# Kernel optimization log

Hardware: AMD Instinct MI355X
Metric: run time of the kernel (lower is better)

The kernel has to match this reference:

```python
import jax, jax.numpy as jnp
import numpy as np
import math

B, H, W = 32, 512, 512
BS = 8
QUALITY = 50.0  # __scale_quality(75) = 200 - 2*75


def _make_dctmtx(bs=BS):
    m = np.empty((bs, bs), dtype=np.float32)
    for j in range(bs):
        for i in range(bs):
            if i == 0:
                m[i, j] = 1.0 / math.sqrt(bs)
            else:
                m[i, j] = math.sqrt(2.0 / bs) * math.cos(math.pi * (2 * j + 1) * i / (2 * bs))
    return jnp.asarray(m)


def _make_quantize():
    qY = np.array([[16,11,10,16,24,40,51,61],[12,12,14,19,26,58,60,55],
                   [14,13,16,24,40,57,69,56],[14,17,22,29,51,87,80,62],
                   [18,22,37,56,68,109,103,77],[24,35,55,64,81,104,113,92],
                   [49,64,78,87,103,121,120,101],[72,92,95,98,112,100,103,99]], dtype=np.float32) / 255.0
    qC = np.array([[17,18,24,47,99,99,99,99],[18,21,26,66,99,99,99,99],
                   [24,26,56,99,99,99,99,99],[47,66,99,99,99,99,99,99],
                   [99,99,99,99,99,99,99,99],[99,99,99,99,99,99,99,99],
                   [99,99,99,99,99,99,99,99],[99,99,99,99,99,99,99,99]], dtype=np.float32) / 255.0
    return jnp.asarray(np.stack([qY, qC, qC], axis=0))


def setup_inputs() -> dict:
    key = jax.random.key(0)
    x = jax.random.uniform(key, (B, 3, H, W), dtype=jnp.float32)
    return {"input": x, "quantize": _make_quantize(), "dctmtx": _make_dctmtx()}


def reference(input, quantize, dctmtx):
    bs = BS
    b, c, h, w = input.shape
    dt = input.dtype
    rgb = 255.0 * input
    # rgb -> ycbcr (3x3 color transform, offset cb/cr by 128, clamp)
    xf = jnp.array([[0.299, 0.587, 0.114],
                    [-0.168735892, -0.331264108, 0.5],
                    [0.5, -0.418687589, -0.081312411]], dtype=dt)
    off = jnp.array([0.0, 128.0, 128.0], dtype=dt)[None, :, None, None]
    ycbcr = jnp.clip(jnp.einsum('bchw,kc->bkhw', rgb, xf) + off, 0.0, 255.0)
    # 2x2 chroma subsample: replace Cb/Cr by 2x2 block means (Y untouched)
    yc = ycbcr[:, :1]
    cc = ycbcr[:, 1:].reshape(b, 2, h // 2, 2, w // 2, 2)
    cm = jnp.mean(cc, axis=(3, 5), keepdims=True)
    cc = jnp.broadcast_to(cm, cc.shape).reshape(b, 2, h, w)
    sample = jnp.concatenate([yc, cc], axis=1) - 128.0
    # extract 8x8 blocks -> [b, h/bs, w/bs, 3, bs, bs]
    blocks = sample.reshape(b, 3, h // bs, bs, w // bs, bs).transpose(0, 2, 4, 1, 3, 5)
    # 2D DCT: D @ X @ D^T
    dcts = jnp.einsum('ij,bhwcjk,lk->bhwcil', dctmtx, blocks, dctmtx)
    # quality-scaled quant table (broadcasts [3,8,8] over blocks)
    q = jnp.round(jnp.clip(jnp.round((jnp.round(quantize * 255.0) * QUALITY + 50.0) / 100.0), 1.0, 255.0))
    comp = jnp.round(dcts / q)
    decomp = jnp.round(comp * jax.lax.stop_gradient(q))
    # IDCT: D^T @ X @ D
    idcts = jnp.einsum('ji,bhwcjk,kl->bhwcil', dctmtx, decomp, dctmtx)
    # merge blocks back -> [b,3,h,w]
    ycbcr2 = idcts.transpose(0, 3, 1, 4, 2, 5).reshape(b, 3, h, w) + 128.0
    # ycbcr -> rgb
    xf2 = jnp.array([[1.0, 0.0, 1.402],
                     [1.0, -0.344136286, -0.714136286],
                     [1.0, 1.772, 0.0]], dtype=dt)
    im = ycbcr2 - off
    rgb2 = jnp.clip(jnp.einsum('bchw,kc->bkhw', im, xf2), 0.0, 255.0)
    return jnp.round(rgb2) / 255.0
```

## Files before the change

kernel.cpp:

```cpp
#include <hip/hip_runtime.h>

#define IN_H 512
#define IN_W 512


__global__ __launch_bounds__(256, 2) void jpeg_kernel(
    const float* __restrict__ in, const float* __restrict__ qz,
    const float* __restrict__ dmtx, float* __restrict__ out)
{
    __shared__ __align__(16) unsigned char smem[39168];
    double*  Ys  = (double*) (smem);
    double*  CbS = (double*) (smem + 17408);
    double*  CrS = (double*) (smem + 22016);
    float*   Vt  = (float*)  (smem + 26624);
    double2* qt  = (double2*)(smem + 35328);
    double*  Dd  = (double*) (smem + 38784);
    float*   Dh  = (float*)  (smem + 39040);

    const int t   = threadIdx.x;
    const int blk = blockIdx.x;
    const int b   = blk >> 7;
    const int rr  = blk & 127;
    const int row0 = (rr >> 1) << 3;
    const int col0 = (rr & 1) << 8;
    const int chs = IN_H * IN_W;

    if (t < 192) {
        const int c = t >> 6, i = (t >> 3) & 7, l = t & 7;
        double v  = (double)qz[t];
        double t1 = rint((rint(v * 255.0) * 50.0 + 50.0) / 100.0);
        double q  = fmin(fmax(t1, 1.0), 255.0);
        qt[(c * 8 + l) * 9 + i] = make_double2(1.0 / q, q);
    }
    if (t < 32) {
        float dv = dmtx[(t >> 2) * 8 + (t & 3)];
        Dd[t] = (double)dv;
        Dh[t] = dv;
    }

    const int s  = t >> 6;
    const int c4 = t & 63;
    {
        const int base = ((b * 3) * IN_H + row0 + 2 * s) * IN_W + col0 + 4 * c4;
        float4 ra = *(const float4*)(in + base);
        float4 rb = *(const float4*)(in + base + IN_W);
        float4 ga = *(const float4*)(in + base + chs);
        float4 gb = *(const float4*)(in + base + chs + IN_W);
        float4 ba = *(const float4*)(in + base + 2 * chs);
        float4 bb = *(const float4*)(in + base + 2 * chs + IN_W);

        float rA[2][4] = {{ra.x,ra.y,ra.z,ra.w},{rb.x,rb.y,rb.z,rb.w}};
        float gA[2][4] = {{ga.x,ga.y,ga.z,ga.w},{gb.x,gb.y,gb.z,gb.w}};
        float bA[2][4] = {{ba.x,ba.y,ba.z,ba.w},{bb.x,bb.y,bb.z,bb.w}};

        double yv[2][4], cbv[2][4], crv[2][4];
        #pragma unroll
        for (int p = 0; p < 2; ++p) {
            #pragma unroll
            for (int k = 0; k < 4; ++k) {
                double R = 255.0 * (double)rA[p][k];
                double G = 255.0 * (double)gA[p][k];
                double B = 255.0 * (double)bA[p][k];
                double y  =  0.299*R + 0.587*G + 0.114*B;
                double cb = -0.168735892*R - 0.331264108*G + 0.5*B + 128.0;
                double cr =  0.5*R - 0.418687589*G - 0.081312411*B + 128.0;
                yv[p][k]  = fmin(fmax(y , 0.0), 255.0) - 128.0;
                cbv[p][k] = fmin(fmax(cb, 0.0), 255.0);
                crv[p][k] = fmin(fmax(cr, 0.0), 255.0);
            }
        }
        const int tile = c4 >> 1, half = c4 & 1;
        #pragma unroll
        for (int p = 0; p < 2; ++p) {
            double* yp = &Ys[tile * 68 + (2*s + p) * 8 + 4 * half];
            *(double2*)(yp)     = make_double2(yv[p][0], yv[p][1]);
            *(double2*)(yp + 2) = make_double2(yv[p][2], yv[p][3]);
        }
        double m0 = (cbv[0][0]+cbv[0][1]+cbv[1][0]+cbv[1][1])*0.25 - 128.0;
        double m1 = (cbv[0][2]+cbv[0][3]+cbv[1][2]+cbv[1][3])*0.25 - 128.0;
        *(double2*)&CbS[tile * 18 + s * 4 + 2 * half] = make_double2(m0, m1);
        double n0 = (crv[0][0]+crv[0][1]+crv[1][0]+crv[1][1])*0.25 - 128.0;
        double n1 = (crv[0][2]+crv[0][3]+crv[1][2]+crv[1][3])*0.25 - 128.0;
        *(double2*)&CrS[tile * 18 + s * 4 + 2 * half] = make_double2(n0, n1);
    }
    __syncthreads();

    const int q8 = t >> 3;
    const int l  = t & 7;
    double dl0, dl1, dl2, dl3;
    {
        double2 dA = *(const double2*)&Dd[l * 4];
        double2 dB = *(const double2*)&Dd[l * 4 + 2];
        dl0 = dA.x; dl1 = dA.y; dl2 = dB.x; dl3 = dB.y;
    }
    const double sgn  = (l & 1) ? -1.0 : 1.0;
    const double dl01 = dl0 + dl1, dl23 = dl2 + dl3;
    const float4* dh4p = (const float4*)Dh;
    float4 d0 = dh4p[0], d1 = dh4p[1], d2 = dh4p[2], d3 = dh4p[3];
    float4 d4 = dh4p[4], d5 = dh4p[5], d6 = dh4p[6], d7 = dh4p[7];

    float acc[3][8];
    float* vtw = &Vt[q8 * 68];

    #pragma unroll
    for (int c = 0; c < 3; ++c) {
        double e2[4], o2[4];
        if (c == 0) {
            const double* base = &Ys[q8 * 68];
            #pragma unroll
            for (int m = 0; m < 4; ++m) {
                double tp[2];
                #pragma unroll
                for (int h = 0; h < 2; ++h) {
                    const double* p = base + (h ? (7 - m) : m) * 8;
                    double2 a0 = *(const double2*)(p);
                    double2 a1 = *(const double2*)(p + 2);
                    double2 a2 = *(const double2*)(p + 4);
                    double2 a3 = *(const double2*)(p + 6);
                    double v0 = fma(sgn, a3.y, a0.x);
                    double v1 = fma(sgn, a3.x, a0.y);
                    double v2 = fma(sgn, a2.y, a1.x);
                    double v3 = fma(sgn, a2.x, a1.y);
                    tp[h] = dl0*v0 + dl1*v1 + dl2*v2 + dl3*v3;
                }
                e2[m] = tp[0] + tp[1];
                o2[m] = tp[0] - tp[1];
            }
        } else {
            const double* base = ((c == 1) ? CbS : CrS) + q8 * 18;
            double u4[4];
            #pragma unroll
            for (int j2 = 0; j2 < 4; ++j2) {
                double2 a0 = *(const double2*)(base + j2 * 4);
                double2 a1 = *(const double2*)(base + j2 * 4 + 2);
                u4[j2] = dl01 * fma(sgn, a1.y, a0.x) + dl23 * fma(sgn, a1.x, a0.y);
            }
            e2[0] = e2[1] = u4[0] + u4[3];  o2[0] = o2[1] = u4[0] - u4[3];
            e2[2] = e2[3] = u4[1] + u4[2];  o2[2] = o2[3] = u4[1] - u4[2];
        }

        float zo[8];
        {
            const double2* dd2  = (const double2*)Dd;
            const double2* qrow = &qt[(c * 8 + l) * 9];
            #pragma unroll
            for (int i = 0; i < 8; ++i) {
                double2 dA = dd2[i * 2], dB = dd2[i * 2 + 1];
                double a64 = (i & 1)
                    ? dA.x*o2[0] + dA.y*o2[1] + dB.x*o2[2] + dB.y*o2[3]
                    : dA.x*e2[0] + dA.y*e2[1] + dB.x*e2[2] + dB.y*e2[3];
                double2 qe = qrow[i];
                zo[i] = (float)(rint(a64 * qe.x) * qe.y);
            }
        }

        float u[8];
        {
            float se0 = zo[0]*d0.x + zo[2]*d2.x + zo[4]*d4.x + zo[6]*d6.x;
            float se1 = zo[0]*d0.y + zo[2]*d2.y + zo[4]*d4.y + zo[6]*d6.y;
            float se2 = zo[0]*d0.z + zo[2]*d2.z + zo[4]*d4.z + zo[6]*d6.z;
            float se3 = zo[0]*d0.w + zo[2]*d2.w + zo[4]*d4.w + zo[6]*d6.w;
            float so0 = zo[1]*d1.x + zo[3]*d3.x + zo[5]*d5.x + zo[7]*d7.x;
            float so1 = zo[1]*d1.y + zo[3]*d3.y + zo[5]*d5.y + zo[7]*d7.y;
            float so2 = zo[1]*d1.z + zo[3]*d3.z + zo[5]*d5.z + zo[7]*d7.z;
            float so3 = zo[1]*d1.w + zo[3]*d3.w + zo[5]*d5.w + zo[7]*d7.w;
            u[0]=se0+so0; u[7]=se0-so0;
            u[1]=se1+so1; u[6]=se1-so1;
            u[2]=se2+so2; u[5]=se2-so2;
            u[3]=se3+so3; u[4]=se3-so3;
        }

        #pragma unroll
        for (int x = 0; x < 8; ++x) vtw[x * 8 + l] = u[x];
        __builtin_amdgcn_wave_barrier();
        float w2[8];
        {
            const float* vr = vtw + l * 8;
            float4 wa = *(const float4*)(vr);
            float4 wb = *(const float4*)(vr + 4);
            w2[0]=wa.x; w2[1]=wa.y; w2[2]=wa.z; w2[3]=wa.w;
            w2[4]=wb.x; w2[5]=wb.y; w2[6]=wb.z; w2[7]=wb.w;
        }
        __builtin_amdgcn_wave_barrier();

        {
            float re0 = w2[0]*d0.x + w2[2]*d2.x + w2[4]*d4.x + w2[6]*d6.x;
            float re1 = w2[0]*d0.y + w2[2]*d2.y + w2[4]*d4.y + w2[6]*d6.y;
            float re2 = w2[0]*d0.z + w2[2]*d2.z + w2[4]*d4.z + w2[6]*d6.z;
            float re3 = w2[0]*d0.w + w2[2]*d2.w + w2[4]*d4.w + w2[6]*d6.w;
            float ro0 = w2[1]*d1.x + w2[3]*d3.x + w2[5]*d5.x + w2[7]*d7.x;
            float ro1 = w2[1]*d1.y + w2[3]*d3.y + w2[5]*d5.y + w2[7]*d7.y;
            float ro2 = w2[1]*d1.z + w2[3]*d3.z + w2[5]*d5.z + w2[7]*d7.z;
            float ro3 = w2[1]*d1.w + w2[3]*d3.w + w2[5]*d5.w + w2[7]*d7.w;
            acc[c][0]=re0+ro0; acc[c][7]=re0-ro0;
            acc[c][1]=re1+ro1; acc[c][6]=re1-ro1;
            acc[c][2]=re2+ro2; acc[c][5]=re2-ro2;
            acc[c][3]=re3+ro3; acc[c][4]=re3-ro3;
        }
    }

    {
        const int obase = ((b * 3) * IN_H + row0 + l) * IN_W + col0 + q8 * 8;
        float R4[8], G4[8], B4[8];
        #pragma unroll
        for (int y = 0; y < 8; ++y) {
            float im0 = acc[0][y] + 128.0f;
            float im1 = acc[1][y];
            float im2 = acc[2][y];
            float R  = fminf(fmaxf(im0 + 1.402f*im2, 0.0f), 255.0f);
            float G  = fminf(fmaxf(im0 - 0.344136286f*im1 - 0.714136286f*im2, 0.0f), 255.0f);
            float Bv = fminf(fmaxf(im0 + 1.772f*im1, 0.0f), 255.0f);
            R4[y] = rintf(R)  * (1.0f/255.0f);
            G4[y] = rintf(G)  * (1.0f/255.0f);
            B4[y] = rintf(Bv) * (1.0f/255.0f);
        }
        *(float4*)(out + obase)               = make_float4(R4[0],R4[1],R4[2],R4[3]);
        *(float4*)(out + obase + 4)           = make_float4(R4[4],R4[5],R4[6],R4[7]);
        *(float4*)(out + obase + chs)         = make_float4(G4[0],G4[1],G4[2],G4[3]);
        *(float4*)(out + obase + chs + 4)     = make_float4(G4[4],G4[5],G4[6],G4[7]);
        *(float4*)(out + obase + 2*chs)       = make_float4(B4[0],B4[1],B4[2],B4[3]);
        *(float4*)(out + obase + 2*chs + 4)   = make_float4(B4[4],B4[5],B4[6],B4[7]);
    }
}

extern "C" void kernel_launch(void* const* d_in, const int* in_sizes, int n_in,
                              void* d_out, int out_size, void* d_ws, size_t ws_size,
                              hipStream_t stream) {
    (void)in_sizes; (void)n_in; (void)out_size; (void)d_ws; (void)ws_size;
    const float* in  = (const float*)d_in[0];
    const float* qz  = (const float*)d_in[1];
    const float* dm  = (const float*)d_in[2];
    float* out = (float*)d_out;
    dim3 grid(4096), blk(256);
    hipLaunchKernelGGL(jpeg_kernel, grid, blk, 0, stream, in, qz, dm, out);
}
```

Baseline: 185.1 us.

## Precompute tables in a prologue kernel and load pixels per row

```diff
diff --git a/kernel.cpp b/kernel.cpp
--- a/kernel.cpp
+++ b/kernel.cpp
@@ -3,152 +3,137 @@
 #define IN_H 512
 #define IN_W 512
 
-
-__global__ __launch_bounds__(256, 2) void jpeg_kernel(
-    const float* __restrict__ in, const float* __restrict__ qz,
-    const float* __restrict__ dmtx, float* __restrict__ out)
+__global__ void jpeg_tables(const float* __restrict__ qz,
+                            const float* __restrict__ dmtx,
+                            double* __restrict__ ws)
 {
-    __shared__ __align__(16) unsigned char smem[39168];
-    double*  Ys  = (double*) (smem);
-    double*  CbS = (double*) (smem + 17408);
-    double*  CrS = (double*) (smem + 22016);
-    float*   Vt  = (float*)  (smem + 26624);
-    double2* qt  = (double2*)(smem + 35328);
-    double*  Dd  = (double*) (smem + 38784);
-    float*   Dh  = (float*)  (smem + 39040);
-
-    const int t   = threadIdx.x;
-    const int blk = blockIdx.x;
-    const int b   = blk >> 7;
-    const int rr  = blk & 127;
-    const int row0 = (rr >> 1) << 3;
-    const int col0 = (rr & 1) << 8;
-    const int chs = IN_H * IN_W;
-
+    const int t = threadIdx.x;
+    if (t < 32) ws[t] = (double)dmtx[(t >> 2) * 8 + (t & 3)];
     if (t < 192) {
         const int c = t >> 6, i = (t >> 3) & 7, l = t & 7;
         double v  = (double)qz[t];
         double t1 = rint((rint(v * 255.0) * 50.0 + 50.0) / 100.0);
         double q  = fmin(fmax(t1, 1.0), 255.0);
-        qt[(c * 8 + l) * 9 + i] = make_double2(1.0 / q, q);
-    }
-    if (t < 32) {
-        float dv = dmtx[(t >> 2) * 8 + (t & 3)];
-        Dd[t] = (double)dv;
-        Dh[t] = dv;
-    }
-
-    const int s  = t >> 6;
-    const int c4 = t & 63;
+        const int idx = (c * 8 + l) * 8 + i;
+        ws[32 + 2 * idx]     = 1.0 / q;
+        ws[32 + 2 * idx + 1] = q;
+    }
+}
+
+__global__ __launch_bounds__(256, 2) void jpeg_kernel(
+    const float* __restrict__ in, const double* __restrict__ ws,
+    float* __restrict__ out)
+{
+    __shared__ __align__(16) double Tq[32 * 68];
+    __shared__ __align__(16) float  Vt[32 * 68];
+
+    const int t    = threadIdx.x;
+    const int tile = t >> 3;
+    const int tl   = t & 7;
+    const int blk  = blockIdx.x;
+    const int b    = blk >> 7;
+    const int rr   = blk & 127;
+    const int row0 = (rr >> 1) << 3;
+    const int col0 = (rr & 1) << 8;
+    const int chs  = IN_H * IN_W;
+
+    double D[8][4];
+    #pragma unroll
+    for (int l = 0; l < 8; ++l)
+        #pragma unroll
+        for (int k = 0; k < 4; ++k) D[l][k] = ws[l * 4 + k];
+    float Dh[8][4];
+    #pragma unroll
+    for (int l = 0; l < 8; ++l)
+        #pragma unroll
+        for (int k = 0; k < 4; ++k) Dh[l][k] = (float)D[l][k];
+
+    double yv[8], hcb[4], hcr[4];
     {
-        const int base = ((b * 3) * IN_H + row0 + 2 * s) * IN_W + col0 + 4 * c4;
-        float4 ra = *(const float4*)(in + base);
-        float4 rb = *(const float4*)(in + base + IN_W);
-        float4 ga = *(const float4*)(in + base + chs);
-        float4 gb = *(const float4*)(in + base + chs + IN_W);
-        float4 ba = *(const float4*)(in + base + 2 * chs);
-        float4 bb = *(const float4*)(in + base + 2 * chs + IN_W);
-
-        float rA[2][4] = {{ra.x,ra.y,ra.z,ra.w},{rb.x,rb.y,rb.z,rb.w}};
-        float gA[2][4] = {{ga.x,ga.y,ga.z,ga.w},{gb.x,gb.y,gb.z,gb.w}};
-        float bA[2][4] = {{ba.x,ba.y,ba.z,ba.w},{bb.x,bb.y,bb.z,bb.w}};
-
-        double yv[2][4], cbv[2][4], crv[2][4];
-        #pragma unroll
-        for (int p = 0; p < 2; ++p) {
-            #pragma unroll
-            for (int k = 0; k < 4; ++k) {
-                double R = 255.0 * (double)rA[p][k];
-                double G = 255.0 * (double)gA[p][k];
-                double B = 255.0 * (double)bA[p][k];
-                double y  =  0.299*R + 0.587*G + 0.114*B;
-                double cb = -0.168735892*R - 0.331264108*G + 0.5*B + 128.0;
-                double cr =  0.5*R - 0.418687589*G - 0.081312411*B + 128.0;
-                yv[p][k]  = fmin(fmax(y , 0.0), 255.0) - 128.0;
-                cbv[p][k] = fmin(fmax(cb, 0.0), 255.0);
-                crv[p][k] = fmin(fmax(cr, 0.0), 255.0);
-            }
-        }
-        const int tile = c4 >> 1, half = c4 & 1;
-        #pragma unroll
-        for (int p = 0; p < 2; ++p) {
-            double* yp = &Ys[tile * 68 + (2*s + p) * 8 + 4 * half];
-            *(double2*)(yp)     = make_double2(yv[p][0], yv[p][1]);
-            *(double2*)(yp + 2) = make_double2(yv[p][2], yv[p][3]);
-        }
-        double m0 = (cbv[0][0]+cbv[0][1]+cbv[1][0]+cbv[1][1])*0.25 - 128.0;
-        double m1 = (cbv[0][2]+cbv[0][3]+cbv[1][2]+cbv[1][3])*0.25 - 128.0;
-        *(double2*)&CbS[tile * 18 + s * 4 + 2 * half] = make_double2(m0, m1);
-        double n0 = (crv[0][0]+crv[0][1]+crv[1][0]+crv[1][1])*0.25 - 128.0;
-        double n1 = (crv[0][2]+crv[0][3]+crv[1][2]+crv[1][3])*0.25 - 128.0;
-        *(double2*)&CrS[tile * 18 + s * 4 + 2 * half] = make_double2(n0, n1);
-    }
-    __syncthreads();
-
-    const int q8 = t >> 3;
-    const int l  = t & 7;
-    double dl0, dl1, dl2, dl3;
-    {
-        double2 dA = *(const double2*)&Dd[l * 4];
-        double2 dB = *(const double2*)&Dd[l * 4 + 2];
-        dl0 = dA.x; dl1 = dA.y; dl2 = dB.x; dl3 = dB.y;
-    }
-    const double sgn  = (l & 1) ? -1.0 : 1.0;
-    const double dl01 = dl0 + dl1, dl23 = dl2 + dl3;
-    const float4* dh4p = (const float4*)Dh;
-    float4 d0 = dh4p[0], d1 = dh4p[1], d2 = dh4p[2], d3 = dh4p[3];
-    float4 d4 = dh4p[4], d5 = dh4p[5], d6 = dh4p[6], d7 = dh4p[7];
+        const float* pin = in + ((b * 3) * IN_H + row0 + tl) * IN_W + col0 + tile * 8;
+        float4 r0 = *(const float4*)(pin);
+        float4 r1 = *(const float4*)(pin + 4);
+        float4 g0 = *(const float4*)(pin + chs);
+        float4 g1 = *(const float4*)(pin + chs + 4);
+        float4 b0 = *(const float4*)(pin + 2 * chs);
+        float4 b1 = *(const float4*)(pin + 2 * chs + 4);
+        float rf[8] = {r0.x,r0.y,r0.z,r0.w,r1.x,r1.y,r1.z,r1.w};
+        float gf[8] = {g0.x,g0.y,g0.z,g0.w,g1.x,g1.y,g1.z,g1.w};
+        float bf[8] = {b0.x,b0.y,b0.z,b0.w,b1.x,b1.y,b1.z,b1.w};
+        #pragma unroll
+        for (int k = 0; k < 8; ++k) {
+            double R = 255.0 * (double)rf[k];
+            double G = 255.0 * (double)gf[k];
+            double B = 255.0 * (double)bf[k];
+            double y  =  0.299*R + 0.587*G + 0.114*B;
+            double cb = -0.168735892*R - 0.331264108*G + 0.5*B + 128.0;
+            double cr =  0.5*R - 0.418687589*G - 0.081312411*B + 128.0;
+            yv[k] = fmin(fmax(y , 0.0), 255.0) - 128.0;
+            cb    = fmin(fmax(cb, 0.0), 255.0) - 128.0;
+            cr    = fmin(fmax(cr, 0.0), 255.0) - 128.0;
+            if ((k & 1) == 0) { hcb[k >> 1] = cb;  hcr[k >> 1] = cr; }
+            else              { hcb[k >> 1] += cb; hcr[k >> 1] += cr; }
+        }
+    }
+
+    double* tp  = &Tq[tile * 68];
+    float*  vp  = &Vt[tile * 68];
+    const double2* qtab = (const double2*)(ws + 32);
 
     float acc[3][8];
-    float* vtw = &Vt[q8 * 68];
 
     #pragma unroll
     for (int c = 0; c < 3; ++c) {
+        double e1[4], o1[4];
+        if (c == 0) {
+            #pragma unroll
+            for (int k = 0; k < 4; ++k) { e1[k] = yv[k] + yv[7-k]; o1[k] = yv[k] - yv[7-k]; }
+        } else {
+            const double* hv = (c == 1) ? hcb : hcr;
+            double A = hv[0] + hv[3], Bv = hv[1] + hv[2];
+            double C = hv[0] - hv[3], E  = hv[1] - hv[2];
+            e1[0] = A; e1[1] = A; e1[2] = Bv; e1[3] = Bv;
+            o1[0] = C; o1[1] = C; o1[2] = E;  o1[3] = E;
+        }
+        double tr[8];
+        #pragma unroll
+        for (int l = 0; l < 8; ++l) {
+            const double* s = (l & 1) ? o1 : e1;
+            tr[l] = D[l][0]*s[0] + D[l][1]*s[1] + D[l][2]*s[2] + D[l][3]*s[3];
+        }
+        #pragma unroll
+        for (int k = 0; k < 4; ++k) {
+            const int s = (2*k + 2*tl) & 7;
+            *(double2*)(tp + tl * 8 + s) = make_double2(tr[2*k], tr[2*k+1]);
+        }
+        __builtin_amdgcn_wave_barrier();
+
+        double colv[8];
+        #pragma unroll
+        for (int j = 0; j < 8; ++j) colv[j] = tp[j * 8 + ((tl + 2*j) & 7)];
+        __builtin_amdgcn_wave_barrier();
+
         double e2[4], o2[4];
         if (c == 0) {
-            const double* base = &Ys[q8 * 68];
             #pragma unroll
-            for (int m = 0; m < 4; ++m) {
-                double tp[2];
-                #pragma unroll
-                for (int h = 0; h < 2; ++h) {
-                    const double* p = base + (h ? (7 - m) : m) * 8;
-                    double2 a0 = *(const double2*)(p);
-                    double2 a1 = *(const double2*)(p + 2);
-                    double2 a2 = *(const double2*)(p + 4);
-                    double2 a3 = *(const double2*)(p + 6);
-                    double v0 = fma(sgn, a3.y, a0.x);
-                    double v1 = fma(sgn, a3.x, a0.y);
-                    double v2 = fma(sgn, a2.y, a1.x);
-                    double v3 = fma(sgn, a2.x, a1.y);
-                    tp[h] = dl0*v0 + dl1*v1 + dl2*v2 + dl3*v3;
-                }
-                e2[m] = tp[0] + tp[1];
-                o2[m] = tp[0] - tp[1];
-            }
+            for (int m = 0; m < 4; ++m) { e2[m] = colv[m] + colv[7-m]; o2[m] = colv[m] - colv[7-m]; }
         } else {
-            const double* base = ((c == 1) ? CbS : CrS) + q8 * 18;
-            double u4[4];
-            #pragma unroll
-            for (int j2 = 0; j2 < 4; ++j2) {
-                double2 a0 = *(const double2*)(base + j2 * 4);
-                double2 a1 = *(const double2*)(base + j2 * 4 + 2);
-                u4[j2] = dl01 * fma(sgn, a1.y, a0.x) + dl23 * fma(sgn, a1.x, a0.y);
-            }
-            e2[0] = e2[1] = u4[0] + u4[3];  o2[0] = o2[1] = u4[0] - u4[3];
-            e2[2] = e2[3] = u4[1] + u4[2];  o2[2] = o2[3] = u4[1] - u4[2];
+            double T0 = 0.25 * (colv[0] + colv[1]);
+            double T1 = 0.25 * (colv[2] + colv[3]);
+            double T2 = 0.25 * (colv[4] + colv[5]);
+            double T3 = 0.25 * (colv[6] + colv[7]);
+            double A = T0 + T3, Bv = T1 + T2, C = T0 - T3, E = T1 - T2;
+            e2[0] = A; e2[1] = A; e2[2] = Bv; e2[3] = Bv;
+            o2[0] = C; o2[1] = C; o2[2] = E;  o2[3] = E;
         }
 
         float zo[8];
         {
-            const double2* dd2  = (const double2*)Dd;
-            const double2* qrow = &qt[(c * 8 + l) * 9];
+            const double2* qrow = qtab + (c * 8 + tl) * 8;
             #pragma unroll
             for (int i = 0; i < 8; ++i) {
-                double2 dA = dd2[i * 2], dB = dd2[i * 2 + 1];
-                double a64 = (i & 1)
-                    ? dA.x*o2[0] + dA.y*o2[1] + dB.x*o2[2] + dB.y*o2[3]
-                    : dA.x*e2[0] + dA.y*e2[1] + dB.x*e2[2] + dB.y*e2[3];
+                const double* s = (i & 1) ? o2 : e2;
+                double a64 = D[i][0]*s[0] + D[i][1]*s[1] + D[i][2]*s[2] + D[i][3]*s[3];
                 double2 qe = qrow[i];
                 zo[i] = (float)(rint(a64 * qe.x) * qe.y);
             }
@@ -156,14 +141,14 @@
 
         float u[8];
         {
-            float se0 = zo[0]*d0.x + zo[2]*d2.x + zo[4]*d4.x + zo[6]*d6.x;
-            float se1 = zo[0]*d0.y + zo[2]*d2.y + zo[4]*d4.y + zo[6]*d6.y;
-            float se2 = zo[0]*d0.z + zo[2]*d2.z + zo[4]*d4.z + zo[6]*d6.z;
-            float se3 = zo[0]*d0.w + zo[2]*d2.w + zo[4]*d4.w + zo[6]*d6.w;
-            float so0 = zo[1]*d1.x + zo[3]*d3.x + zo[5]*d5.x + zo[7]*d7.x;
-            float so1 = zo[1]*d1.y + zo[3]*d3.y + zo[5]*d5.y + zo[7]*d7.y;
-            float so2 = zo[1]*d1.z + zo[3]*d3.z + zo[5]*d5.z + zo[7]*d7.z;
-            float so3 = zo[1]*d1.w + zo[3]*d3.w + zo[5]*d5.w + zo[7]*d7.w;
+            float se0 = zo[0]*Dh[0][0] + zo[2]*Dh[2][0] + zo[4]*Dh[4][0] + zo[6]*Dh[6][0];
+            float se1 = zo[0]*Dh[0][1] + zo[2]*Dh[2][1] + zo[4]*Dh[4][1] + zo[6]*Dh[6][1];
+            float se2 = zo[0]*Dh[0][2] + zo[2]*Dh[2][2] + zo[4]*Dh[4][2] + zo[6]*Dh[6][2];
+            float se3 = zo[0]*Dh[0][3] + zo[2]*Dh[2][3] + zo[4]*Dh[4][3] + zo[6]*Dh[6][3];
+            float so0 = zo[1]*Dh[1][0] + zo[3]*Dh[3][0] + zo[5]*Dh[5][0] + zo[7]*Dh[7][0];
+            float so1 = zo[1]*Dh[1][1] + zo[3]*Dh[3][1] + zo[5]*Dh[5][1] + zo[7]*Dh[7][1];
+            float so2 = zo[1]*Dh[1][2] + zo[3]*Dh[3][2] + zo[5]*Dh[5][2] + zo[7]*Dh[7][2];
+            float so3 = zo[1]*Dh[1][3] + zo[3]*Dh[3][3] + zo[5]*Dh[5][3] + zo[7]*Dh[7][3];
             u[0]=se0+so0; u[7]=se0-so0;
             u[1]=se1+so1; u[6]=se1-so1;
             u[2]=se2+so2; u[5]=se2-so2;
@@ -171,27 +156,26 @@
         }
 
         #pragma unroll
-        for (int x = 0; x < 8; ++x) vtw[x * 8 + l] = u[x];
+        for (int x = 0; x < 8; ++x) vp[x * 8 + tl] = u[x];
         __builtin_amdgcn_wave_barrier();
         float w2[8];
         {
-            const float* vr = vtw + l * 8;
-            float4 wa = *(const float4*)(vr);
-            float4 wb = *(const float4*)(vr + 4);
+            float4 wa = *(const float4*)(vp + tl * 8);
+            float4 wb = *(const float4*)(vp + tl * 8 + 4);
             w2[0]=wa.x; w2[1]=wa.y; w2[2]=wa.z; w2[3]=wa.w;
             w2[4]=wb.x; w2[5]=wb.y; w2[6]=wb.z; w2[7]=wb.w;
         }
         __builtin_amdgcn_wave_barrier();
 
         {
-            float re0 = w2[0]*d0.x + w2[2]*d2.x + w2[4]*d4.x + w2[6]*d6.x;
-            float re1 = w2[0]*d0.y + w2[2]*d2.y + w2[4]*d4.y + w2[6]*d6.y;
-            float re2 = w2[0]*d0.z + w2[2]*d2.z + w2[4]*d4.z + w2[6]*d6.z;
-            float re3 = w2[0]*d0.w + w2[2]*d2.w + w2[4]*d4.w + w2[6]*d6.w;
-            float ro0 = w2[1]*d1.x + w2[3]*d3.x + w2[5]*d5.x + w2[7]*d7.x;
-            float ro1 = w2[1]*d1.y + w2[3]*d3.y + w2[5]*d5.y + w2[7]*d7.y;
-            float ro2 = w2[1]*d1.z + w2[3]*d3.z + w2[5]*d5.z + w2[7]*d7.z;
-            float ro3 = w2[1]*d1.w + w2[3]*d3.w + w2[5]*d5.w + w2[7]*d7.w;
+            float re0 = w2[0]*Dh[0][0] + w2[2]*Dh[2][0] + w2[4]*Dh[4][0] + w2[6]*Dh[6][0];
+            float re1 = w2[0]*Dh[0][1] + w2[2]*Dh[2][1] + w2[4]*Dh[4][1] + w2[6]*Dh[6][1];
+            float re2 = w2[0]*Dh[0][2] + w2[2]*Dh[2][2] + w2[4]*Dh[4][2] + w2[6]*Dh[6][2];
+            float re3 = w2[0]*Dh[0][3] + w2[2]*Dh[2][3] + w2[4]*Dh[4][3] + w2[6]*Dh[6][3];
+            float ro0 = w2[1]*Dh[1][0] + w2[3]*Dh[3][0] + w2[5]*Dh[5][0] + w2[7]*Dh[7][0];
+            float ro1 = w2[1]*Dh[1][1] + w2[3]*Dh[3][1] + w2[5]*Dh[5][1] + w2[7]*Dh[7][1];
+            float ro2 = w2[1]*Dh[1][2] + w2[3]*Dh[3][2] + w2[5]*Dh[5][2] + w2[7]*Dh[7][2];
+            float ro3 = w2[1]*Dh[1][3] + w2[3]*Dh[3][3] + w2[5]*Dh[5][3] + w2[7]*Dh[7][3];
             acc[c][0]=re0+ro0; acc[c][7]=re0-ro0;
             acc[c][1]=re1+ro1; acc[c][6]=re1-ro1;
             acc[c][2]=re2+ro2; acc[c][5]=re2-ro2;
@@ -200,7 +184,7 @@
     }
 
     {
-        const int obase = ((b * 3) * IN_H + row0 + l) * IN_W + col0 + q8 * 8;
+        const int obase = ((b * 3) * IN_H + row0 + tl) * IN_W + col0 + tile * 8;
         float R4[8], G4[8], B4[8];
         #pragma unroll
         for (int y = 0; y < 8; ++y) {
@@ -214,23 +198,25 @@
             G4[y] = rintf(G)  * (1.0f/255.0f);
             B4[y] = rintf(Bv) * (1.0f/255.0f);
         }
-        *(float4*)(out + obase)               = make_float4(R4[0],R4[1],R4[2],R4[3]);
-        *(float4*)(out + obase + 4)           = make_float4(R4[4],R4[5],R4[6],R4[7]);
-        *(float4*)(out + obase + chs)         = make_float4(G4[0],G4[1],G4[2],G4[3]);
-        *(float4*)(out + obase + chs + 4)     = make_float4(G4[4],G4[5],G4[6],G4[7]);
-        *(float4*)(out + obase + 2*chs)       = make_float4(B4[0],B4[1],B4[2],B4[3]);
-        *(float4*)(out + obase + 2*chs + 4)   = make_float4(B4[4],B4[5],B4[6],B4[7]);
+        *(float4*)(out + obase)             = make_float4(R4[0],R4[1],R4[2],R4[3]);
+        *(float4*)(out + obase + 4)         = make_float4(R4[4],R4[5],R4[6],R4[7]);
+        *(float4*)(out + obase + chs)       = make_float4(G4[0],G4[1],G4[2],G4[3]);
+        *(float4*)(out + obase + chs + 4)   = make_float4(G4[4],G4[5],G4[6],G4[7]);
+        *(float4*)(out + obase + 2*chs)     = make_float4(B4[0],B4[1],B4[2],B4[3]);
+        *(float4*)(out + obase + 2*chs + 4) = make_float4(B4[4],B4[5],B4[6],B4[7]);
     }
 }
 
 extern "C" void kernel_launch(void* const* d_in, const int* in_sizes, int n_in,
                               void* d_out, int out_size, void* d_ws, size_t ws_size,
                               hipStream_t stream) {
-    (void)in_sizes; (void)n_in; (void)out_size; (void)d_ws; (void)ws_size;
+    (void)in_sizes; (void)n_in; (void)out_size; (void)ws_size;
     const float* in  = (const float*)d_in[0];
     const float* qz  = (const float*)d_in[1];
     const float* dm  = (const float*)d_in[2];
+    double* ws = (double*)d_ws;
     float* out = (float*)d_out;
-    dim3 grid(4096), blk(256);
-    hipLaunchKernelGGL(jpeg_kernel, grid, blk, 0, stream, in, qz, dm, out);
+    hipLaunchKernelGGL(jpeg_tables, dim3(1), dim3(256), 0, stream, qz, dm, ws);
+    hipLaunchKernelGGL(jpeg_kernel, dim3(4096), dim3(256), 0, stream,
+                       in, (const double*)ws, out);
 }
```

After: 211.4 us. 1.14x slower.
